# Performance work log

Hardware: AMD Instinct MI355X
Metric: run time of the kernel (lower is better)

The kernel has to match this reference:

```python
import jax, jax.numpy as jnp
import numpy as np

B, S, D = 8, 1024, 1024
NH, DH = 16, 64  # d_head = d_model // n_heads
NEG = -1e9


def setup_inputs() -> dict:
    key = jax.random.key(0)
    ks = jax.random.split(key, 10)
    H = jax.random.normal(ks[0], (B, S, D), dtype=jnp.float32)
    mask = jax.random.randint(ks[1], (B, S, S), 0, 2, dtype=jnp.int32)
    # Stacked per-head Linear weights (torch Linear: y = x @ W.T + b, W is [out,in])
    w = 0.02
    Wq = jax.random.normal(ks[2], (NH, DH, DH), dtype=jnp.float32) * w
    bq = jnp.zeros((NH, DH), dtype=jnp.float32)
    Wk = jax.random.normal(ks[3], (NH, DH, DH), dtype=jnp.float32) * w
    bk = jnp.zeros((NH, DH), dtype=jnp.float32)
    Wv = jax.random.normal(ks[4], (NH, DH, DH), dtype=jnp.float32) * w
    bv = jnp.zeros((NH, DH), dtype=jnp.float32)
    Wo = jax.random.normal(ks[5], (D, D), dtype=jnp.float32) * w
    bo = jnp.zeros((D,), dtype=jnp.float32)
    return {"H": H, "mask": mask, "Wq": Wq, "bq": bq, "Wk": Wk, "bk": bk,
            "Wv": Wv, "bv": bv, "Wo": Wo, "bo": bo}


def reference(H, mask, Wq, bq, Wk, bk, Wv, bv, Wo, bo):
    # torch.split(H, d_head, -1) == reshape to (B, S, NH, DH): head h sees slice h
    Hh = H.reshape(B, S, NH, DH)
    # per-head linear projections, batched over heads (W is [out,in] -> contract on in)
    Q = jnp.einsum('bsnd,ned->bsne', Hh, Wq) + bq  # (B,S,NH,DH)
    K = jnp.einsum('bsnd,ned->bsne', Hh, Wk) + bk
    V = jnp.einsum('bsnd,ned->bsne', Hh, Wv) + bv
    scale = np.sqrt(DH).astype(np.float32)
    scores = jnp.einsum('bsne,btne->nbst', Q, K) / scale  # (NH,B,S,S)
    scores = jnp.where(mask[None] == 0, jnp.float32(NEG), scores)
    A = jax.nn.softmax(scores, axis=-1)  # dropout is identity in eval mode
    heads = jnp.einsum('nbst,btnd->bsnd', A, V)  # (B,S,NH,DH)
    concat = heads.reshape(B, S, D)
    output = concat @ Wo.T + bo
    return output, A  # A: stacked per-head attention matrices (NH,B,S,S)
```

## Files before the change

kernel.cpp:

```cpp
#include <hip/hip_runtime.h>
#include <hip/hip_bf16.h>

typedef __bf16 v8bf __attribute__((ext_vector_type(8)));
typedef __bf16 v4bf __attribute__((ext_vector_type(4)));
typedef short v4ss __attribute__((ext_vector_type(4)));
typedef float v4f __attribute__((ext_vector_type(4)));

constexpr int B_ = 8, S_ = 1024, D_ = 1024, NH_ = 16, DH_ = 64;
constexpr float NEGV = -1e9f;

#define MFMA(a, b, c) __builtin_amdgcn_mfma_f32_16x16x32_bf16((a), (b), (c), 0, 0, 0)

__device__ __forceinline__ v4f mfma_k16(v4bf a, v4bf b, v4f c) {
#if __has_builtin(__builtin_amdgcn_mfma_f32_16x16x16bf16_1k)
  return __builtin_amdgcn_mfma_f32_16x16x16bf16_1k(
      __builtin_bit_cast(v4ss, a), __builtin_bit_cast(v4ss, b), c, 0, 0, 0);
#elif __has_builtin(__builtin_amdgcn_mfma_f32_16x16x16_bf16)
  return __builtin_amdgcn_mfma_f32_16x16x16_bf16(a, b, c, 0, 0, 0);
#else
  v4f d;
  asm volatile("v_mfma_f32_16x16x16_bf16 %0, %1, %2, %3\n\ts_nop 7\n\ts_nop 7"
               : "=v"(d)
               : "v"(a), "v"(b), "v"(c));
  return d;
#endif
}

__device__ __forceinline__ __bf16 tobf(float f) {
  unsigned u = __float_as_uint(f);
  u += 0x7fffu + ((u >> 16) & 1);
  unsigned short s = (unsigned short)(u >> 16);
  return __builtin_bit_cast(__bf16, s);
}

__device__ __forceinline__ v8bf cvt8(float4 a, float4 b) {
  v8bf r;
  r[0] = tobf(a.x); r[1] = tobf(a.y); r[2] = tobf(a.z); r[3] = tobf(a.w);
  r[4] = tobf(b.x); r[5] = tobf(b.y); r[6] = tobf(b.z); r[7] = tobf(b.w);
  return r;
}

typedef __attribute__((address_space(3))) unsigned lds_uint;
typedef __attribute__((address_space(1))) unsigned gbl_uint;
__device__ __forceinline__ void gload_lds16(const void* g, void* l) {
  __builtin_amdgcn_global_load_lds((const gbl_uint*)g, (lds_uint*)l, 16, 0, 0);
}

__device__ __forceinline__ void stage_k(const __bf16* Kb, int chunk, char* buf,
                                        int wave, int lane) {
  const char* src = (const char*)(Kb + (size_t)chunk * 64 * DH_);
#pragma unroll
  for (int h = 0; h < 2; ++h) {
    int i = wave * 128 + h * 64 + lane;
    int row = i >> 3, cd = i & 7;
    const char* g = src + row * 128 + ((cd ^ (row & 7)) << 4);
    char* l = buf + (wave * 2048 + h * 1024);
    gload_lds16(g, l);
  }
}

__device__ __forceinline__ v8bf lds_k(const char* buf, int row, int gc) {
  return *(const v8bf*)(buf + row * 128 + ((gc ^ (row & 7)) << 4));
}

__device__ __forceinline__ void vload(v4bf* dst, const __bf16* Vb, int ct,
                                      int quad, int col) {
#pragma unroll
  for (int d = 0; d < 4; ++d)
    dst[d] = *(const v4bf*)(Vb + (size_t)(d * 16 + col) * S_ + ct * 16 + quad * 4);
}

__global__ __launch_bounds__(256) void maskpack(const int* __restrict__ mask,
                                                unsigned long long* __restrict__ bits) {
  size_t base = (size_t)blockIdx.x * 256;
  int m = mask[base + threadIdx.x];
  unsigned long long w = __ballot(m != 0);
  if ((threadIdx.x & 63) == 0) bits[base / 64 + (threadIdx.x >> 6)] = w;
}

__global__ __launch_bounds__(256) void wpack(const float* __restrict__ Wq,
                                             const float* __restrict__ Wk,
                                             const float* __restrict__ Wv,
                                             const float* __restrict__ Wo,
                                             __bf16* __restrict__ dst) {
  int i = blockIdx.x * 256 + threadIdx.x;
  float v;
  if (i < 65536) v = Wq[i];
  else if (i < 131072) v = Wk[i - 65536];
  else if (i < 196608) v = Wv[i - 131072];
  else v = Wo[i - 196608];
  dst[i] = tobf(v);
}

__global__ __launch_bounds__(256) void qkv_mfma(
    const float* __restrict__ H, const __bf16* __restrict__ Wb,
    const float* __restrict__ bq, const float* __restrict__ bk,
    const float* __restrict__ bv,
    __bf16* __restrict__ Q, __bf16* __restrict__ K, __bf16* __restrict__ Vt) {
  int idx = blockIdx.x;
  int rt = idx & 15, n = (idx >> 4) & 15, b = idx >> 8;
  int tid = threadIdx.x, wave = tid >> 6, lane = tid & 63;
  int quad = lane >> 4, col = lane & 15;
  int s0 = rt * 64 + wave * 16;

  const float* Hrow = H + ((size_t)(b * S_ + s0 + col)) * D_ + n * DH_;
  v8bf af[2];
#pragma unroll
  for (int ks = 0; ks < 2; ks++) {
    const float* p = Hrow + ks * 32 + quad * 8;
    af[ks] = cvt8(*(const float4*)p, *(const float4*)(p + 4));
  }

  const __bf16* Wm[3] = {Wb + n * 4096, Wb + 65536 + n * 4096,
                         Wb + 131072 + n * 4096};
  const float* Bm[3] = {bq + n * 64, bk + n * 64, bv + n * 64};
  __bf16* Qdst = Q + ((size_t)(b * NH_ + n) * S_) * DH_;
  __bf16* Kdst = K + ((size_t)(b * NH_ + n) * S_) * DH_;
  __bf16* Vdst = Vt + ((size_t)(b * NH_ + n) * DH_) * S_;

#pragma unroll
  for (int w = 0; w < 3; w++) {
#pragma unroll
    for (int ct = 0; ct < 4; ct++) {
      int e = ct * 16 + col;
      v4f acc = {0.f, 0.f, 0.f, 0.f};
#pragma unroll
      for (int ks = 0; ks < 2; ks++) {
        const __bf16* p = Wm[w] + (size_t)e * 64 + ks * 32 + quad * 8;
        acc = MFMA(af[ks], *(const v8bf*)p, acc);
      }
      float bias = Bm[w][e];
      if (w == 0) {
#pragma unroll
        for (int g = 0; g < 4; g++)
          Qdst[(size_t)(s0 + quad * 4 + g) * DH_ + e] =
              tobf((acc[g] + bias) * 0.125f);
      } else if (w == 1) {
#pragma unroll
        for (int g = 0; g < 4; g++)
          Kdst[(size_t)(s0 + quad * 4 + g) * DH_ + e] = tobf(acc[g] + bias);
      } else {
#pragma unroll
        for (int g = 0; g < 4; g++)
          Vdst[(size_t)e * S_ + s0 + quad * 4 + g] = tobf(acc[g] + bias);
      }
    }
  }
}

__global__ __launch_bounds__(256, 4) void attn_pv(
    const __bf16* __restrict__ Q, const __bf16* __restrict__ K,
    const __bf16* __restrict__ Vt, const unsigned long long* __restrict__ mbits,
    float* __restrict__ A, __bf16* __restrict__ X) {
  __shared__ __align__(16) char kbuf[2][64 * 128];

  int idx = blockIdx.x;
  int n = idx & 15, st = (idx >> 4) & 15, b = idx >> 8;
  int tid = threadIdx.x, wave = tid >> 6, lane = tid & 63;
  int quad = lane >> 4, col = lane & 15;
  int s0 = st * 64 + wave * 16;

  const __bf16* Qb = Q + ((size_t)(b * NH_ + n) * S_ + s0 + col) * DH_;
  v8bf qf0 = *(const v8bf*)(Qb + quad * 8);
  v8bf qf1 = *(const v8bf*)(Qb + 32 + quad * 8);

  const __bf16* Kb = K + ((size_t)(b * NH_ + n) * S_) * DH_;
  const __bf16* Vb = Vt + ((size_t)(b * NH_ + n) * DH_) * S_;
  const unsigned long long* mrow = mbits + ((size_t)b * S_ + s0 + col) * (S_ / 64);

  int shb = quad * 4;
  float mx = -INFINITY, l = 0.f;

  stage_k(Kb, 0, kbuf[0], wave, lane);
  unsigned long long mw = mrow[0], mwn = 0;

  for (int c = 0; c < 16; ++c) {
    __syncthreads();
    if (c + 1 < 16) {
      stage_k(Kb, c + 1, kbuf[(c + 1) & 1], wave, lane);
      mwn = mrow[c + 1];
    } else {
      mwn = mw;
    }
    const char* buf = kbuf[c & 1];
#pragma unroll
    for (int tl = 0; tl < 4; ++tl) {
      int row = tl * 16 + col;
      v4f acc = {0.f, 0.f, 0.f, 0.f};
      acc = MFMA(lds_k(buf, row, quad), qf0, acc);
      acc = MFMA(lds_k(buf, row, quad + 4), qf1, acc);
      int sh = tl * 16 + shb;
      float v0 = ((mw >> (sh + 0)) & 1ull) ? acc[0] : NEGV;
      float v1 = ((mw >> (sh + 1)) & 1ull) ? acc[1] : NEGV;
      float v2 = ((mw >> (sh + 2)) & 1ull) ? acc[2] : NEGV;
      float v3 = ((mw >> (sh + 3)) & 1ull) ? acc[3] : NEGV;
      float vm = fmaxf(fmaxf(v0, v1), fmaxf(v2, v3));
      float mnew = fmaxf(mx, vm);
      float e = __expf(v0 - mnew) + __expf(v1 - mnew) +
                __expf(v2 - mnew) + __expf(v3 - mnew);
      l = l * __expf(mx - mnew) + e;
      mx = mnew;
    }
    mw = mwn;
  }

#pragma unroll
  for (int off = 16; off < 64; off <<= 1) {
    float mo = __shfl_xor(mx, off);
    float lo = __shfl_xor(l, off);
    float M = fmaxf(mx, mo);
    l = l * __expf(mx - M) + lo * __expf(mo - M);
    mx = M;
  }
  float inv = 1.f / l;

  float* Ab = A + (((size_t)n * B_ + b) * S_ + s0 + col) * S_;
  v4f opv[4];
#pragma unroll
  for (int d = 0; d < 4; ++d) opv[d] = {0.f, 0.f, 0.f, 0.f};

  stage_k(Kb, 0, kbuf[0], wave, lane);
  v4bf vb0[4], vb1[4];
  vload(vb0, Vb, 0, quad, col);
  unsigned long long mw2 = mrow[0], mwn2 = 0;

  for (int c = 0; c < 16; ++c) {
    __syncthreads();
    if (c + 1 < 16) {
      stage_k(Kb, c + 1, kbuf[(c + 1) & 1], wave, lane);
      mwn2 = mrow[c + 1];
    } else {
      mwn2 = mw2;
    }
    const char* buf = kbuf[c & 1];
#pragma unroll
    for (int tl = 0; tl < 4; ++tl) {
      int ct = c * 4 + tl;
      v4bf* vcur = (tl & 1) ? vb1 : vb0;
      v4bf* vnext = (tl & 1) ? vb0 : vb1;
      if (ct + 1 < 64) vload(vnext, Vb, ct + 1, quad, col);
      int row = tl * 16 + col;
      v4f acc = {0.f, 0.f, 0.f, 0.f};
      acc = MFMA(lds_k(buf, row, quad), qf0, acc);
      acc = MFMA(lds_k(buf, row, quad + 4), qf1, acc);
      int sh = tl * 16 + shb;
      v4f av;
      v4bf pb;
#pragma unroll
      for (int g = 0; g < 4; ++g) {
        float e = __expf(acc[g] - mx) * inv;
        float a = ((mw2 >> (sh + g)) & 1ull) ? e : 0.f;
        av[g] = a;
        pb[g] = tobf(a);
      }
      __builtin_nontemporal_store(av, (v4f*)(Ab + ct * 16 + quad * 4));
#pragma unroll
      for (int d = 0; d < 4; ++d) opv[d] = mfma_k16(pb, vcur[d], opv[d]);
    }
    mw2 = mwn2;
  }

#pragma unroll
  for (int d = 0; d < 4; ++d)
#pragma unroll
    for (int g = 0; g < 4; ++g)
      X[((size_t)(b * S_ + s0 + quad * 4 + g)) * D_ + n * 64 + d * 16 + col] =
          tobf(opv[d][g]);
}

__global__ __launch_bounds__(256) void oproj_mfma(
    const __bf16* __restrict__ X, const __bf16* __restrict__ Wob,
    const float* __restrict__ bo, float* __restrict__ out) {
  int idx = blockIdx.x;
  int nt = idx & 15, mt = idx >> 4;
  int tid = threadIdx.x, wave = tid >> 6, lane = tid & 63;
  int quad = lane >> 4, col = lane & 15;
  int m0 = mt * 64 + wave * 16, o0 = nt * 64;

  const __bf16* Xb = X + (size_t)(m0 + col) * D_;

  v4f acc[4];
#pragma unroll
  for (int ct = 0; ct < 4; ct++) acc[ct] = {0.f, 0.f, 0.f, 0.f};

  for (int k0 = 0; k0 < D_; k0 += 32) {
    v8bf a8 = *(const v8bf*)(Xb + k0 + quad * 8);
#pragma unroll
    for (int ct = 0; ct < 4; ct++) {
      const __bf16* p = Wob + (size_t)(o0 + ct * 16 + col) * D_ + k0 + quad * 8;
      acc[ct] = MFMA(a8, *(const v8bf*)p, acc[ct]);
    }
  }
#pragma unroll
  for (int ct = 0; ct < 4; ct++) {
    int o = o0 + ct * 16 + col;
    float bias = bo[o];
#pragma unroll
    for (int g = 0; g < 4; g++)
      __builtin_nontemporal_store(
          acc[ct][g] + bias, &out[(size_t)(m0 + quad * 4 + g) * D_ + o]);
  }
}

extern "C" void kernel_launch(void* const* d_in, const int* in_sizes, int n_in,
                              void* d_out, int out_size, void* d_ws,
                              size_t ws_size, hipStream_t stream) {
  const float* H = (const float*)d_in[0];
  const int* mask = (const int*)d_in[1];
  const float* Wq = (const float*)d_in[2];
  const float* bq = (const float*)d_in[3];
  const float* Wk = (const float*)d_in[4];
  const float* bk = (const float*)d_in[5];
  const float* Wv = (const float*)d_in[6];
  const float* bv = (const float*)d_in[7];
  const float* Wo = (const float*)d_in[8];
  const float* bo = (const float*)d_in[9];

  float* out = (float*)d_out;
  float* A = out + (size_t)B_ * S_ * D_;

  const size_t qkv_elems = (size_t)B_ * NH_ * S_ * DH_;
  unsigned long long* mbits = (unsigned long long*)d_ws;
  __bf16* Q = (__bf16*)(mbits + (size_t)B_ * S_ * (S_ / 64));
  __bf16* K = Q + qkv_elems;
  __bf16* Vt = K + qkv_elems;
  __bf16* X = Vt + qkv_elems;
  __bf16* Wb = X + qkv_elems;
  __bf16* Wob = Wb + 196608;

  wpack<<<4864, 256, 0, stream>>>(Wq, Wk, Wv, Wo, Wb);
  maskpack<<<B_ * S_ * (S_ / 256), 256, 0, stream>>>(mask, mbits);
  qkv_mfma<<<B_ * NH_ * (S_ / 64), 256, 0, stream>>>(H, Wb, bq, bk, bv, Q, K, Vt);
  attn_pv<<<B_ * (S_ / 64) * NH_, 256, 0, stream>>>(Q, K, Vt, mbits, A, X);
  oproj_mfma<<<(B_ * S_ / 64) * (D_ / 64), 256, 0, stream>>>(X, Wob, bo, out);
}
```

Measured before the change: 990.6 us.

## Stage weight and activation tiles through LDS in projection kernels

```diff
diff --git a/kernel.cpp b/kernel.cpp
--- a/kernel.cpp
+++ b/kernel.cpp
@@ -46,14 +46,13 @@
   __builtin_amdgcn_global_load_lds((const gbl_uint*)g, (lds_uint*)l, 16, 0, 0);
 }
 
-__device__ __forceinline__ void stage_k(const __bf16* Kb, int chunk, char* buf,
-                                        int wave, int lane) {
-  const char* src = (const char*)(Kb + (size_t)chunk * 64 * DH_);
+__device__ __forceinline__ void stage_tile(const char* src, size_t stride,
+                                           char* buf, int wave, int lane) {
 #pragma unroll
   for (int h = 0; h < 2; ++h) {
     int i = wave * 128 + h * 64 + lane;
     int row = i >> 3, cd = i & 7;
-    const char* g = src + row * 128 + ((cd ^ (row & 7)) << 4);
+    const char* g = src + (size_t)row * stride + ((cd ^ (row & 7)) << 4);
     char* l = buf + (wave * 2048 + h * 1024);
     gload_lds16(g, l);
   }
@@ -97,12 +96,18 @@
     const float* __restrict__ bq, const float* __restrict__ bk,
     const float* __restrict__ bv,
     __bf16* __restrict__ Q, __bf16* __restrict__ K, __bf16* __restrict__ Vt) {
+  __shared__ __align__(16) char wlds[3][64 * 128];
+
   int idx = blockIdx.x;
   int rt = idx & 15, n = (idx >> 4) & 15, b = idx >> 8;
   int tid = threadIdx.x, wave = tid >> 6, lane = tid & 63;
   int quad = lane >> 4, col = lane & 15;
   int s0 = rt * 64 + wave * 16;
 
+  stage_tile((const char*)(Wb + n * 4096), 128, wlds[0], wave, lane);
+  stage_tile((const char*)(Wb + 65536 + n * 4096), 128, wlds[1], wave, lane);
+  stage_tile((const char*)(Wb + 131072 + n * 4096), 128, wlds[2], wave, lane);
+
   const float* Hrow = H + ((size_t)(b * S_ + s0 + col)) * D_ + n * DH_;
   v8bf af[2];
 #pragma unroll
@@ -111,24 +116,21 @@
     af[ks] = cvt8(*(const float4*)p, *(const float4*)(p + 4));
   }
 
-  const __bf16* Wm[3] = {Wb + n * 4096, Wb + 65536 + n * 4096,
-                         Wb + 131072 + n * 4096};
   const float* Bm[3] = {bq + n * 64, bk + n * 64, bv + n * 64};
   __bf16* Qdst = Q + ((size_t)(b * NH_ + n) * S_) * DH_;
   __bf16* Kdst = K + ((size_t)(b * NH_ + n) * S_) * DH_;
   __bf16* Vdst = Vt + ((size_t)(b * NH_ + n) * DH_) * S_;
 
+  __syncthreads();
+
 #pragma unroll
   for (int w = 0; w < 3; w++) {
 #pragma unroll
     for (int ct = 0; ct < 4; ct++) {
       int e = ct * 16 + col;
       v4f acc = {0.f, 0.f, 0.f, 0.f};
-#pragma unroll
-      for (int ks = 0; ks < 2; ks++) {
-        const __bf16* p = Wm[w] + (size_t)e * 64 + ks * 32 + quad * 8;
-        acc = MFMA(af[ks], *(const v8bf*)p, acc);
-      }
+      acc = MFMA(af[0], lds_k(wlds[w], e, quad), acc);
+      acc = MFMA(af[1], lds_k(wlds[w], e, quad + 4), acc);
       float bias = Bm[w][e];
       if (w == 0) {
 #pragma unroll
@@ -140,9 +142,10 @@
         for (int g = 0; g < 4; g++)
           Kdst[(size_t)(s0 + quad * 4 + g) * DH_ + e] = tobf(acc[g] + bias);
       } else {
-#pragma unroll
-        for (int g = 0; g < 4; g++)
-          Vdst[(size_t)e * S_ + s0 + quad * 4 + g] = tobf(acc[g] + bias);
+        v4bf pv;
+#pragma unroll
+        for (int g = 0; g < 4; g++) pv[g] = tobf(acc[g] + bias);
+        *(v4bf*)(Vdst + (size_t)e * S_ + s0 + quad * 4) = pv;
       }
     }
   }
@@ -171,13 +174,14 @@
   int shb = quad * 4;
   float mx = -INFINITY, l = 0.f;
 
-  stage_k(Kb, 0, kbuf[0], wave, lane);
+  stage_tile((const char*)Kb, 128, kbuf[0], wave, lane);
   unsigned long long mw = mrow[0], mwn = 0;
 
   for (int c = 0; c < 16; ++c) {
     __syncthreads();
     if (c + 1 < 16) {
-      stage_k(Kb, c + 1, kbuf[(c + 1) & 1], wave, lane);
+      stage_tile((const char*)(Kb + (size_t)(c + 1) * 64 * DH_), 128,
+                 kbuf[(c + 1) & 1], wave, lane);
       mwn = mrow[c + 1];
     } else {
       mwn = mw;
@@ -219,7 +223,7 @@
 #pragma unroll
   for (int d = 0; d < 4; ++d) opv[d] = {0.f, 0.f, 0.f, 0.f};
 
-  stage_k(Kb, 0, kbuf[0], wave, lane);
+  stage_tile((const char*)Kb, 128, kbuf[0], wave, lane);
   v4bf vb0[4], vb1[4];
   vload(vb0, Vb, 0, quad, col);
   unsigned long long mw2 = mrow[0], mwn2 = 0;
@@ -227,7 +231,8 @@
   for (int c = 0; c < 16; ++c) {
     __syncthreads();
     if (c + 1 < 16) {
-      stage_k(Kb, c + 1, kbuf[(c + 1) & 1], wave, lane);
+      stage_tile((const char*)(Kb + (size_t)(c + 1) * 64 * DH_), 128,
+                 kbuf[(c + 1) & 1], wave, lane);
       mwn2 = mrow[c + 1];
     } else {
       mwn2 = mw2;
@@ -271,24 +276,41 @@
 __global__ __launch_bounds__(256) void oproj_mfma(
     const __bf16* __restrict__ X, const __bf16* __restrict__ Wob,
     const float* __restrict__ bo, float* __restrict__ out) {
+  __shared__ __align__(16) char xbuf[2][64 * 128];
+  __shared__ __align__(16) char wbuf[2][64 * 128];
+
   int idx = blockIdx.x;
   int nt = idx & 15, mt = idx >> 4;
   int tid = threadIdx.x, wave = tid >> 6, lane = tid & 63;
   int quad = lane >> 4, col = lane & 15;
-  int m0 = mt * 64 + wave * 16, o0 = nt * 64;
-
-  const __bf16* Xb = X + (size_t)(m0 + col) * D_;
+  int m0b = mt * 64, o0 = nt * 64;
+
+  const char* Xbase = (const char*)(X + (size_t)m0b * D_);
+  const char* Wbase = (const char*)(Wob + (size_t)o0 * D_);
+
+  stage_tile(Xbase, 2048, xbuf[0], wave, lane);
+  stage_tile(Wbase, 2048, wbuf[0], wave, lane);
 
   v4f acc[4];
 #pragma unroll
   for (int ct = 0; ct < 4; ct++) acc[ct] = {0.f, 0.f, 0.f, 0.f};
 
-  for (int k0 = 0; k0 < D_; k0 += 32) {
-    v8bf a8 = *(const v8bf*)(Xb + k0 + quad * 8);
+  for (int s = 0; s < 16; ++s) {
+    __syncthreads();
+    if (s + 1 < 16) {
+      stage_tile(Xbase + (s + 1) * 128, 2048, xbuf[(s + 1) & 1], wave, lane);
+      stage_tile(Wbase + (s + 1) * 128, 2048, wbuf[(s + 1) & 1], wave, lane);
+    }
+    const char* xb = xbuf[s & 1];
+    const char* wb = wbuf[s & 1];
+    int mrow = wave * 16 + col;
+    v8bf a0 = lds_k(xb, mrow, quad);
+    v8bf a1 = lds_k(xb, mrow, quad + 4);
 #pragma unroll
     for (int ct = 0; ct < 4; ct++) {
-      const __bf16* p = Wob + (size_t)(o0 + ct * 16 + col) * D_ + k0 + quad * 8;
-      acc[ct] = MFMA(a8, *(const v8bf*)p, acc[ct]);
+      int orow = ct * 16 + col;
+      acc[ct] = MFMA(a0, lds_k(wb, orow, quad), acc[ct]);
+      acc[ct] = MFMA(a1, lds_k(wb, orow, quad + 4), acc[ct]);
     }
   }
 #pragma unroll
@@ -298,7 +320,8 @@
 #pragma unroll
     for (int g = 0; g < 4; g++)
       __builtin_nontemporal_store(
-          acc[ct][g] + bias, &out[(size_t)(m0 + quad * 4 + g) * D_ + o]);
+          acc[ct][g] + bias,
+          &out[(size_t)(m0b + wave * 16 + quad * 4 + g) * D_ + o]);
   }
 }
 
```

Measured after the change: 873.2 us. 11.8% less time.
